# Kernel tuning notes

Measured on AMD Instinct MI355X. Metric: run time of the kernel, lower is better.

Reference implementation:

```python
import jax, jax.numpy as jnp
import numpy as np
from functools import partial

WIDTH = 2560
LRU = 2560
HEADS = 8
DCONV = 4
B = 4
L = 2048


def setup_inputs() -> dict:
    key = jax.random.key(0)
    ks = jax.random.split(key, 16)
    bw = LRU // HEADS
    x = jax.random.normal(ks[0], (B, L, WIDTH), dtype=jnp.float32)
    segment_pos = jnp.broadcast_to(jnp.arange(L, dtype=jnp.int32), (B, L))
    # indices of the last DCONV frames of the left-padded conv input (length L+DCONV-1)
    base = (jnp.arange(DCONV, dtype=jnp.int32) + (L - 1))
    conv_idx = jnp.broadcast_to(base, (B, LRU, DCONV))
    s = 0.02
    return {
        "x": x,
        "segment_pos": segment_pos,
        "conv_idx": conv_idx,
        "Wx": jax.random.normal(ks[1], (LRU, WIDTH), jnp.float32) * s,
        "bx": jax.random.normal(ks[2], (LRU,), jnp.float32) * s,
        "Wy": jax.random.normal(ks[3], (LRU, WIDTH), jnp.float32) * s,
        "conv_w": jax.random.normal(ks[4], (LRU, DCONV), jnp.float32) * s,  # depthwise kernel
        "conv_b": jax.random.normal(ks[5], (LRU,), jnp.float32) * s,
        "gx_w": jax.random.normal(ks[6], (HEADS, bw, bw), jnp.float32) * s,
        "gx_b": jax.random.normal(ks[7], (HEADS, bw), jnp.float32) * s,
        "ga_w": jax.random.normal(ks[8], (HEADS, bw, bw), jnp.float32) * s,
        "ga_b": jax.random.normal(ks[9], (HEADS, bw), jnp.float32) * s,
        "a_param": jax.random.normal(ks[10], (LRU,), jnp.float32),
        "y_bias": jax.random.normal(ks[11], (1, 1, LRU), jnp.float32) * s,
        "Wout": jax.random.normal(ks[12], (WIDTH, LRU), jnp.float32) * s,
        "bout": jax.random.normal(ks[13], (WIDTH,), jnp.float32) * s,
    }


def _block_diag(x, w):
    # x: [B,L,(h*i)], w: [h,i,j] -> [B,L,(h*j)]
    b, l, _ = x.shape
    h, bw, _ = w.shape
    xb = x.reshape(b, l, h, bw)
    y = jnp.einsum('blhi,hij->blhj', xb, w)
    return y.reshape(b, l, h * bw)


def _scan_op(c1, c2):
    a1, b1 = c1
    a2, b2 = c2
    return (a1 * a2, a2 * b1 + b2)


def reference(x, segment_pos, conv_idx, Wx, bx, Wy, conv_w, conv_b,
              gx_w, gx_b, ga_w, ga_b, a_param, y_bias, Wout, bout):
    dc = conv_w.shape[1]
    seqlen = x.shape[1]

    y = jnp.einsum('bld,ed->ble', x, Wy)                 # linear_y (no bias)
    xl = jnp.einsum('bld,ed->ble', x, Wx) + bx           # linear_x

    # causal depthwise conv1d, padding dc-1 on the left, keep first seqlen
    xpad = jnp.pad(xl, ((0, 0), (dc - 1, 0), (0, 0)))    # [B, L+dc-1, LRU]
    xc = conv_b + sum(conv_w[:, k] * xpad[:, k:k + seqlen, :] for k in range(dc))

    # conv_state: gather of padded (channels-first) input at conv_idx
    conv_state = jnp.take_along_axis(xpad.transpose(0, 2, 1), conv_idx.astype(jnp.int32), axis=2)

    gx = _block_diag(xc, gx_w)  # fuse_bias=True: bias added inside rg_lru
    ga = _block_diag(xc, ga_w)

    # rg_lru_ref
    reset = (segment_pos == 0).astype(x.dtype)[..., None]        # [B,L,1]
    gate_x = jax.nn.sigmoid(gx + gx_b.reshape(-1))
    gate_a = jax.nn.sigmoid(ga + ga_b.reshape(-1))
    c = -8.0 * jax.nn.softplus(a_param)
    log_a = c * gate_a
    a = jnp.exp(log_a) * (1.0 - reset)
    multiplier = jnp.sqrt(1.0 - jnp.exp(2.0 * log_a))
    multiplier = reset + (1.0 - reset) * multiplier
    normalized_x = xc * gate_x * multiplier

    _, h = jax.lax.associative_scan(_scan_op, (a, normalized_x), axis=1)
    last_h = h[:, -1]

    out = h * jax.nn.gelu(y + y_bias, approximate=False)
    out = jnp.einsum('ble,de->bld', out, Wout) + bout    # linear_out
    return out, conv_state, last_h
```

## Files before the change

### kernel.cpp

```cpp
#include <hip/hip_runtime.h>
#include <hip/hip_bf16.h>

#define WIDTH_ 2560
#define LRU_   2560
#define HEADS_ 8
#define BW_    320
#define DCONV_ 4
#define BB     4
#define LL     2048
#define MROWS  (BB*LL)
#define NCH    32
#define CLEN   (LL/NCH)

typedef unsigned short ushort_t;
typedef __attribute__((ext_vector_type(8))) short short8;
typedef __attribute__((ext_vector_type(4))) float f32x4;

__device__ __forceinline__ unsigned short f2bf(float f) {
  union { float f; unsigned u; } v; v.f = f;
  unsigned r = v.u + 0x7fffu + ((v.u >> 16) & 1u);
  return (unsigned short)(r >> 16);
}
__device__ __forceinline__ float bf2f(unsigned short h) {
  union { unsigned u; float f; } v; v.u = ((unsigned)h) << 16;
  return v.f;
}
__device__ __forceinline__ void async_load16(const void* g, void* l) {
  __builtin_amdgcn_global_load_lds(
      (const __attribute__((address_space(1))) unsigned*)g,
      (__attribute__((address_space(3))) unsigned*)l, 16, 0, 0);
}
__device__ __forceinline__ float sigmoidf_(float x) {
  return 1.f / (1.f + __expf(-x));
}
__device__ __forceinline__ size_t pkaddr(int e, int m, int PL) {
  return ((size_t)(e >> 3) * PL + m) * 8 + (e & 7);
}

__global__ void tp_pack(const float* __restrict__ src, ushort_t* __restrict__ dst,
                        int R, int C, int PL, int RO) {
  __shared__ float tile[64][65];
  const int r0 = blockIdx.x * 64, c0 = blockIdx.y * 64;
  const int t = threadIdx.x;
#pragma unroll
  for (int it = 0; it < 4; ++it) {
    int row = it * 16 + (t >> 4);
    int col = (t & 15) * 4;
    *(float4*)&tile[row][col] = *(const float4*)&src[(size_t)(r0 + row) * C + c0 + col];
  }
  __syncthreads();
#pragma unroll
  for (int it = 0; it < 2; ++it) {
    int c8 = it * 4 + (t >> 6);
    int m  = t & 63;
    ushort_t o[8];
#pragma unroll
    for (int j = 0; j < 8; ++j) o[j] = f2bf(tile[m][c8 * 8 + j]);
    *(short8*)&dst[((size_t)(c0 / 8 + c8) * PL + RO + r0 + m) * 8] = *(short8*)o;
  }
}

__global__ void gw_pack(const float* __restrict__ w, ushort_t* __restrict__ dst,
                        int RO, int n_) {
  int i = blockIdx.x * blockDim.x + threadIdx.x;
  if (i >= n_) return;
  int n = i % BW_;
  int k = (i / BW_) % BW_;
  int h = i / (BW_ * BW_);
  dst[((size_t)(h * 40 + (k >> 3)) * 640 + RO + n) * 8 + (k & 7)] =
      f2bf(w[((size_t)h * BW_ + k) * BW_ + n]);
}

__global__ void ctab_kernel(const float* __restrict__ apar, float* __restrict__ ctab) {
  int e = blockIdx.x * blockDim.x + threadIdx.x;
  if (e >= LRU_) return;
  float ap = apar[e];
  float sp = (ap > 15.f) ? ap : log1pf(expf(ap));
  ctab[e] = -8.f * sp;
}

template<int EPI>
__global__ __launch_bounds__(512, 2)
void gemm_pk(const ushort_t* __restrict__ A,
             const ushort_t* __restrict__ B, int NPL,
             void* __restrict__ C0, void* __restrict__ C1,
             const float* __restrict__ bias) {
  constexpr int NT = 80;
  __shared__ char smem[131072];
  const int tid = threadIdx.x;
  const int lane = tid & 63, w = tid >> 6;
  const int wr = w >> 2, wc = w & 3;
  const int l15 = lane & 15, l4 = lane >> 4;

  const int nblk = gridDim.x;
  const int TN = nblk >> 5;
  const int x8 = blockIdx.x & 7, c = blockIdx.x >> 3;
  const int tm = (x8 * 4 + c / TN) * 256;
  const int tn = (c % TN) * 256;

  const char* aS[2]; const char* bS[2]; int ld[2];
#pragma unroll
  for (int u = 0; u < 2; ++u) {
    int lb = (u * 512 + tid) * 16;
    int slot = lb >> 12, m = (lb >> 4) & 255;
    aS[u] = (const char*)A + ((size_t)slot * MROWS + tm + m) * 16;
    bS[u] = (const char*)B + ((size_t)slot * NPL + tn + m) * 16;
    ld[u] = lb;
  }
  const size_t aStep = (size_t)4 * MROWS * 16;
  const size_t bStep = (size_t)4 * NPL * 16;

  f32x4 acc[8][4] = {};

#pragma unroll
  for (int kt = 0; kt < 3; ++kt)
#pragma unroll
    for (int u = 0; u < 2; ++u) {
      async_load16(aS[u] + kt * aStep, smem + kt * 16384 + ld[u]);
      async_load16(bS[u] + kt * bStep, smem + 65536 + kt * 16384 + ld[u]);
    }

  const int aRd = l4 * 4096 + (wr * 128 + l15) * 16;
  const int bRd = 65536 + l4 * 4096 + (wc * 64 + l15) * 16;

  for (int t = 0; t < NT; ++t) {
    if (t < NT - 2)       asm volatile("s_waitcnt vmcnt(8)" ::: "memory");
    else if (t == NT - 2) asm volatile("s_waitcnt vmcnt(4)" ::: "memory");
    else                  asm volatile("s_waitcnt vmcnt(0)" ::: "memory");
    __builtin_amdgcn_s_barrier();
    if (t + 3 < NT) {
      const int kt = t + 3, p = kt & 3;
#pragma unroll
      for (int u = 0; u < 2; ++u) {
        async_load16(aS[u] + kt * aStep, smem + p * 16384 + ld[u]);
        async_load16(bS[u] + kt * bStep, smem + 65536 + p * 16384 + ld[u]);
      }
    }
    const char* base = smem + (t & 3) * 16384;
    short8 bfrag[4], afrag[4];
#pragma unroll
    for (int nf = 0; nf < 4; ++nf)
      bfrag[nf] = *(const short8*)(base + bRd + nf * 256);
#pragma unroll
    for (int mf = 0; mf < 4; ++mf)
      afrag[mf] = *(const short8*)(base + aRd + mf * 256);
    __builtin_amdgcn_s_setprio(1);
#pragma unroll
    for (int mf = 0; mf < 4; ++mf)
#pragma unroll
      for (int nf = 0; nf < 4; ++nf)
        acc[mf][nf] = __builtin_amdgcn_mfma_f32_16x16x32_bf16(
            afrag[mf], bfrag[nf], acc[mf][nf], 0, 0, 0);
    __builtin_amdgcn_s_setprio(0);
#pragma unroll
    for (int mf = 0; mf < 4; ++mf)
      afrag[mf] = *(const short8*)(base + aRd + 1024 + mf * 256);
    __builtin_amdgcn_s_setprio(1);
#pragma unroll
    for (int mf = 0; mf < 4; ++mf)
#pragma unroll
      for (int nf = 0; nf < 4; ++nf)
        acc[4 + mf][nf] = __builtin_amdgcn_mfma_f32_16x16x32_bf16(
            afrag[mf], bfrag[nf], acc[4 + mf][nf], 0, 0, 0);
    __builtin_amdgcn_s_setprio(0);
  }

  const int crow0 = tm + wr * 128 + l4 * 4;
  const int ccol0 = tn + wc * 64 + l15;
#pragma unroll
  for (int m = 0; m < 8; ++m)
#pragma unroll
    for (int n = 0; n < 4; ++n) {
      const int col = ccol0 + n * 16;
#pragma unroll
      for (int r = 0; r < 4; ++r) {
        const int row = crow0 + m * 16 + r;
        float v = acc[m][n][r];
        if (EPI == 0) {
          ((float*)C0)[(size_t)row * 2560 + col] = v + bias[col];
        } else {
          if (col < 2560)
            ((ushort_t*)C0)[pkaddr(col, row, MROWS)] = f2bf(v + bias[col]);
          else
            ((ushort_t*)C1)[pkaddr(col - 2560, row, MROWS)] = f2bf(v);
        }
      }
    }
}

__global__ __launch_bounds__(256, 2)
void gate_gemm(const ushort_t* __restrict__ A,
               const ushort_t* __restrict__ Bw,
               ushort_t* __restrict__ GX,
               ushort_t* __restrict__ AAo,
               const float* __restrict__ gxb, const float* __restrict__ gab,
               const float* __restrict__ ctab, const int* __restrict__ seg) {
  constexpr int BM = 128, BN = 64, NF = 2;
  __shared__ char smem[12288];
  const int tid = threadIdx.x;
  const int w = tid >> 6, lane = tid & 63;
  const int wr = w >> 1, wc = w & 1;
  const int l15 = lane & 15, l4 = lane >> 4;
  const int tm = blockIdx.x * BM;
  const int tn = blockIdx.y * BN;
  const int z = blockIdx.z;

  const char* aS[2]; int lda_[2];
#pragma unroll
  for (int u = 0; u < 2; ++u) {
    int lb = (u * 256 + tid) * 16;
    int slot = lb >> 11, m = (lb >> 4) & 127;
    aS[u] = (const char*)A + ((size_t)(z * 40 + slot) * MROWS + tm + m) * 16;
    lda_[u] = lb;
  }
  const char* bS; int ldb_;
  {
    int lb = tid * 16;
    int slot = lb >> 10, n = (lb >> 4) & 63;
    bS = (const char*)Bw + ((size_t)(z * 40 + slot) * 640 + tn + n) * 16;
    ldb_ = 8192 + lb;
  }
  const size_t aStep = (size_t)4 * MROWS * 16;
  const size_t bStep = (size_t)4 * 640 * 16;

  f32x4 acc[4][NF] = {};
  const int aRd = l4 * 2048 + (wr * 64 + l15) * 16;
  const int bRd = 8192 + l4 * 1024 + (wc * 32 + l15) * 16;

  for (int kt = 0; kt < 10; ++kt) {
#pragma unroll
    for (int u = 0; u < 2; ++u)
      async_load16(aS[u] + kt * aStep, smem + lda_[u]);
    async_load16(bS + kt * bStep, smem + ldb_);
    __syncthreads();
    short8 af[4], bfr[NF];
#pragma unroll
    for (int mf = 0; mf < 4; ++mf)
      af[mf] = *(const short8*)(smem + aRd + mf * 256);
#pragma unroll
    for (int nf = 0; nf < NF; ++nf)
      bfr[nf] = *(const short8*)(smem + bRd + nf * 256);
#pragma unroll
    for (int mf = 0; mf < 4; ++mf)
#pragma unroll
      for (int nf = 0; nf < NF; ++nf)
        acc[mf][nf] = __builtin_amdgcn_mfma_f32_16x16x32_bf16(af[mf], bfr[nf], acc[mf][nf], 0, 0, 0);
    __syncthreads();
  }

  const int crow0 = tm + wr * 64 + l4 * 4;
  const int ccol0 = tn + wc * 32 + l15;
#pragma unroll
  for (int mf = 0; mf < 4; ++mf) {
#pragma unroll
    for (int nf = 0; nf < NF; ++nf) {
      const int cih = ccol0 + nf * 16;
#pragma unroll
      for (int r = 0; r < 4; ++r) {
        const int row = crow0 + mf * 16 + r;
        if (cih < BW_) {
          const int gc = z * BW_ + cih;
          float v = acc[mf][nf][r] + gxb[gc];
          float xc = bf2f(A[pkaddr(gc, row, MROWS)]);
          GX[pkaddr(gc, row, MROWS)] = f2bf(xc * sigmoidf_(v));
        } else {
          const int gc = z * BW_ + cih - BW_;
          float v = acc[mf][nf][r] + gab[gc];
          float la = ctab[gc] * sigmoidf_(v);
          float av = (seg[row] == 0) ? 0.f : expf(la);
          AAo[pkaddr(gc, row, MROWS)] = f2bf(av);
        }
      }
    }
  }
}

__global__ void conv_pk(const ushort_t* __restrict__ xl, const float* __restrict__ convw,
                        const float* __restrict__ convb, ushort_t* __restrict__ xc) {
  int i = blockIdx.x * blockDim.x + threadIdx.x;
  if (i >= 320 * MROWS) return;
  int m = i % MROWS;
  int p = i / MROWS;
  int t = m % LL;
  const ushort_t* pl = xl + (size_t)p * MROWS * 8;
  short8 v0 = {}, v1 = {}, v2 = {}, v3;
  v3 = *(const short8*)(pl + (size_t)m * 8);
  if (t >= 1) v2 = *(const short8*)(pl + (size_t)(m - 1) * 8);
  if (t >= 2) v1 = *(const short8*)(pl + (size_t)(m - 2) * 8);
  if (t >= 3) v0 = *(const short8*)(pl + (size_t)(m - 3) * 8);
  ushort_t o[8];
#pragma unroll
  for (int u = 0; u < 8; ++u) {
    int e = p * 8 + u;
    float4 wv = ((const float4*)convw)[e];
    float acc = convb[e];
    acc += wv.x * bf2f((ushort_t)v0[u]);
    acc += wv.y * bf2f((ushort_t)v1[u]);
    acc += wv.z * bf2f((ushort_t)v2[u]);
    acc += wv.w * bf2f((ushort_t)v3[u]);
    o[u] = f2bf(acc);
  }
  *(short8*)(xc + (size_t)p * MROWS * 8 + (size_t)m * 8) = *(short8*)o;
}

__global__ void conv_state_kernel(const ushort_t* __restrict__ xl, const int* __restrict__ cidx,
                                  float* __restrict__ cs) {
  int i = blockIdx.x * blockDim.x + threadIdx.x;
  if (i >= BB * LRU_ * DCONV_) return;
  int e = (i / DCONV_) % LRU_;
  int b = i / (DCONV_ * LRU_);
  int idx = cidx[i];
  int ts = idx - (DCONV_ - 1);
  float v = 0.f;
  if (ts >= 0 && ts < LL) v = bf2f(xl[pkaddr(e, b * LL + ts, MROWS)]);
  cs[i] = v;
}

__global__ void scanA(const ushort_t* __restrict__ AA, const ushort_t* __restrict__ GX,
                      float* __restrict__ cA, float* __restrict__ cH) {
  int i = blockIdx.x * blockDim.x + threadIdx.x;
  if (i >= BB * NCH * LRU_) return;
  int e = i % LRU_;
  int c = (i / LRU_) % NCH;
  int b = i / (LRU_ * NCH);
  float Ap = 1.f, h = 0.f;
  size_t base = pkaddr(e, b * LL + c * CLEN, MROWS);
  for (int t = 0; t < CLEN; ++t) {
    size_t j = base + (size_t)t * 8;
    float a = bf2f(AA[j]);
    float nx = bf2f(GX[j]) * sqrtf(fmaxf(0.f, 1.f - a * a));
    Ap *= a;
    h = a * h + nx;
  }
  cA[i] = Ap; cH[i] = h;
}

__global__ void scanB(const float* __restrict__ cA, const float* __restrict__ cH,
                      float* __restrict__ hInit) {
  int i = blockIdx.x * blockDim.x + threadIdx.x;
  if (i >= BB * LRU_) return;
  int e = i % LRU_;
  int b = i / LRU_;
  float h = 0.f;
  for (int c = 0; c < NCH; ++c) {
    size_t j = ((size_t)b * NCH + c) * LRU_ + e;
    hInit[j] = h;
    h = cA[j] * h + cH[j];
  }
}

__global__ void scanC(const ushort_t* __restrict__ AA, const ushort_t* __restrict__ GXpre,
                      const float* __restrict__ hInit, const ushort_t* __restrict__ ybf,
                      const float* __restrict__ ybias, float* __restrict__ lastH) {
  int i = blockIdx.x * blockDim.x + threadIdx.x;
  if (i >= BB * NCH * LRU_) return;
  int e = i % LRU_;
  int c = (i / LRU_) % NCH;
  int b = i / (LRU_ * NCH);
  float h = hInit[i];
  float yb = ybias[e];
  ushort_t* pre = (ushort_t*)GXpre;
  size_t base = pkaddr(e, b * LL + c * CLEN, MROWS);
  for (int t = 0; t < CLEN; ++t) {
    size_t j = base + (size_t)t * 8;
    float a = bf2f(AA[j]);
    float nx = bf2f(GXpre[j]) * sqrtf(fmaxf(0.f, 1.f - a * a));
    h = a * h + nx;
    float yv = bf2f(ybf[j]) + yb;
    float g = 0.5f * yv * (1.f + erff(yv * 0.70710678118f));
    pre[j] = f2bf(h * g);
  }
  if (c == NCH - 1) lastH[(size_t)b * LRU_ + e] = h;
}

extern "C" void kernel_launch(void* const* d_in, const int* in_sizes, int n_in,
                              void* d_out, int out_size, void* d_ws, size_t ws_size,
                              hipStream_t stream) {
  const float* x     = (const float*)d_in[0];
  const int*   seg   = (const int*)d_in[1];
  const int*   cidx  = (const int*)d_in[2];
  const float* Wx    = (const float*)d_in[3];
  const float* bx    = (const float*)d_in[4];
  const float* Wy    = (const float*)d_in[5];
  const float* convw = (const float*)d_in[6];
  const float* convb = (const float*)d_in[7];
  const float* gxw   = (const float*)d_in[8];
  const float* gxb   = (const float*)d_in[9];
  const float* gaw   = (const float*)d_in[10];
  const float* gab   = (const float*)d_in[11];
  const float* apar  = (const float*)d_in[12];
  const float* ybias = (const float*)d_in[13];
  const float* Wout  = (const float*)d_in[14];
  const float* bout  = (const float*)d_in[15];

  float* out    = (float*)d_out;
  float* cs_out = out + (size_t)MROWS * WIDTH_;
  float* lh_out = cs_out + (size_t)BB * LRU_ * DCONV_;

  ushort_t* ybf = (ushort_t*)d_out;
  ushort_t* AA  = (ushort_t*)((char*)d_out + (size_t)41943040);

  const size_t SZ_BIG = (size_t)MROWS * LRU_ * 2;
  const size_t SZ_WC  = (size_t)(2 * LRU_) * WIDTH_ * 2;
  const size_t SZ_GW  = (size_t)HEADS_ * 640 * BW_ * 2;
  const size_t SZ_SM  = (size_t)BB * NCH * LRU_ * 4;
  size_t need = SZ_BIG * 3 + SZ_WC + SZ_GW + 10240 + SZ_SM * 3;
  if (ws_size < need) return;

  char* p = (char*)d_ws;
  ushort_t* xpk   = (ushort_t*)p; p += SZ_BIG;
  ushort_t* wpk   = (ushort_t*)p; p += SZ_WC;
  ushort_t* T2    = (ushort_t*)p; p += SZ_BIG;
  ushort_t* xcbf  = (ushort_t*)p; p += SZ_BIG;
  ushort_t* gwT   = (ushort_t*)p; p += SZ_GW;
  float*    ctab  = (float*)p;    p += 10240;
  float*    cA    = (float*)p;    p += SZ_SM;
  float*    cH    = (float*)p;    p += SZ_SM;
  float*    hInit = (float*)p;    p += SZ_SM;
  ushort_t* woutpk = wpk;

  const int BLK = 256;
  tp_pack<<<dim3(MROWS / 64, WIDTH_ / 64), 256, 0, stream>>>(x, xpk, MROWS, WIDTH_, MROWS, 0);
  tp_pack<<<dim3(LRU_ / 64, WIDTH_ / 64), 256, 0, stream>>>(Wx, wpk, LRU_, WIDTH_, 2 * LRU_, 0);
  tp_pack<<<dim3(LRU_ / 64, WIDTH_ / 64), 256, 0, stream>>>(Wy, wpk, LRU_, WIDTH_, 2 * LRU_, LRU_);

  gemm_pk<1><<<640, 512, 0, stream>>>(xpk, wpk, 2 * LRU_, T2, ybf, bx);

  tp_pack<<<dim3(LRU_ / 64, WIDTH_ / 64), 256, 0, stream>>>(Wout, woutpk, WIDTH_, LRU_, WIDTH_, 0);

  conv_pk<<<(320 * MROWS + BLK - 1) / BLK, BLK, 0, stream>>>(T2, convw, convb, xcbf);
  conv_state_kernel<<<(BB * LRU_ * DCONV_ + BLK - 1) / BLK, BLK, 0, stream>>>(T2, cidx, cs_out);

  gw_pack<<<(HEADS_ * BW_ * BW_ + BLK - 1) / BLK, BLK, 0, stream>>>(gxw, gwT, 0, HEADS_ * BW_ * BW_);
  gw_pack<<<(HEADS_ * BW_ * BW_ + BLK - 1) / BLK, BLK, 0, stream>>>(gaw, gwT, BW_, HEADS_ * BW_ * BW_);
  ctab_kernel<<<(LRU_ + BLK - 1) / BLK, BLK, 0, stream>>>(apar, ctab);

  gate_gemm<<<dim3(MROWS / 128, 10, HEADS_), BLK, 0, stream>>>(
      xcbf, gwT, T2, AA, gxb, gab, ctab, seg);

  scanA<<<(BB * NCH * LRU_ + BLK - 1) / BLK, BLK, 0, stream>>>(AA, T2, cA, cH);
  scanB<<<(BB * LRU_ + BLK - 1) / BLK, BLK, 0, stream>>>(cA, cH, hInit);
  scanC<<<(BB * NCH * LRU_ + BLK - 1) / BLK, BLK, 0, stream>>>(AA, T2, hInit, ybf, ybias, lh_out);

  gemm_pk<0><<<320, 512, 0, stream>>>(T2, woutpk, WIDTH_, out, nullptr, bout);
}
```

Baseline: 591.8 us.

## Restructure big GEMM main loop into 8-phase K=64 double-buffered pipeline

Rewrites the main loop of the 256x256 bf16 GEMM to use K=64 steps, split into half-tiles, with double buffering. Each step runs four phases that interleave LDS fragment reads, async global staging of the next A/B halves, and MFMA bursts, separated by sched_barriers and workgroup barriers. B fragments are reused across the four A-quarter phases. The aim is better overlap of global loads and LDS reads with MFMA and fewer loop iterations, at the cost of more barriers per K-step and more register pressure. The gate_gemm edit only inlines a constant.

```diff
diff --git a/kernel.cpp b/kernel.cpp
--- a/kernel.cpp
+++ b/kernel.cpp
@@ -79,18 +79,59 @@
   ctab[e] = -8.f * sp;
 }
 
+
+#define STG_A(KT, H, BUF) do { \
+  _Pragma("unroll") for (int u_ = 0; u_ < 2; ++u_) \
+    async_load16(Ach + aoff[u_] + (size_t)(KT) * aKt + (H) * 2048, \
+                 smem + ((BUF) * 2 + (H)) * 16384 + ldst[u_]); } while (0)
+#define STG_B(KT, H, BUF) do { \
+  _Pragma("unroll") for (int u_ = 0; u_ < 2; ++u_) \
+    async_load16(Bch + boff[u_] + (size_t)(KT) * bKt + (H) * 2048, \
+                 smem + 65536 + ((BUF) * 2 + (H)) * 16384 + ldst[u_]); } while (0)
+
+#define PHASE(BUF, Q, STAGE_STMT, VMN) do { \
+  __builtin_amdgcn_sched_barrier(0); \
+  const char* Ah_ = smem + ((BUF) * 2 + wr) * 16384; \
+  const char* Bh_ = smem + 65536 + ((BUF) * 2 + (wc >> 1)) * 16384; \
+  if ((Q) == 0) { \
+    _Pragma("unroll") for (int nf = 0; nf < 4; ++nf) \
+      _Pragma("unroll") for (int s = 0; s < 2; ++s) \
+        bfr[nf][s] = *(const short8*)(Bh_ + ((s * 4 + l4) * 128 + brow + nf * 16 + l15) * 16); \
+  } \
+  short8 a_[2][2]; \
+  _Pragma("unroll") for (int mm = 0; mm < 2; ++mm) \
+    _Pragma("unroll") for (int s = 0; s < 2; ++s) \
+      a_[mm][s] = *(const short8*)(Ah_ + ((s * 4 + l4) * 128 + ((Q) * 2 + mm) * 16 + l15) * 16); \
+  STAGE_STMT; \
+  __builtin_amdgcn_sched_barrier(0); \
+  __builtin_amdgcn_s_barrier(); \
+  asm volatile("s_waitcnt lgkmcnt(0)" ::: "memory"); \
+  __builtin_amdgcn_sched_barrier(0); \
+  __builtin_amdgcn_s_setprio(1); \
+  _Pragma("unroll") for (int mm = 0; mm < 2; ++mm) \
+    _Pragma("unroll") for (int nf = 0; nf < 4; ++nf) \
+      _Pragma("unroll") for (int s = 0; s < 2; ++s) \
+        acc[(Q) * 2 + mm][nf] = __builtin_amdgcn_mfma_f32_16x16x32_bf16( \
+            a_[mm][s], bfr[nf][s], acc[(Q) * 2 + mm][nf], 0, 0, 0); \
+  __builtin_amdgcn_s_setprio(0); \
+  if ((VMN) == 4)      asm volatile("s_waitcnt vmcnt(4)" ::: "memory"); \
+  else if ((VMN) == 0) asm volatile("s_waitcnt vmcnt(0)" ::: "memory"); \
+  __builtin_amdgcn_sched_barrier(0); \
+  __builtin_amdgcn_s_barrier(); \
+} while (0)
+
 template<int EPI>
 __global__ __launch_bounds__(512, 2)
 void gemm_pk(const ushort_t* __restrict__ A,
              const ushort_t* __restrict__ B, int NPL,
              void* __restrict__ C0, void* __restrict__ C1,
              const float* __restrict__ bias) {
-  constexpr int NT = 80;
   __shared__ char smem[131072];
   const int tid = threadIdx.x;
   const int lane = tid & 63, w = tid >> 6;
   const int wr = w >> 2, wc = w & 3;
   const int l15 = lane & 15, l4 = lane >> 4;
+  const int brow = (wc & 1) * 64;
 
   const int nblk = gridDim.x;
   const int TN = nblk >> 5;
@@ -98,71 +139,42 @@
   const int tm = (x8 * 4 + c / TN) * 256;
   const int tn = (c % TN) * 256;
 
-  const char* aS[2]; const char* bS[2]; int ld[2];
+  const char* Ach = (const char*)A;
+  const char* Bch = (const char*)B;
+  const size_t aKt = (size_t)8 * MROWS * 16;
+  const size_t bKt = (size_t)8 * NPL * 16;
+
+  size_t aoff[2], boff[2]; int ldst[2];
 #pragma unroll
   for (int u = 0; u < 2; ++u) {
     int lb = (u * 512 + tid) * 16;
-    int slot = lb >> 12, m = (lb >> 4) & 255;
-    aS[u] = (const char*)A + ((size_t)slot * MROWS + tm + m) * 16;
-    bS[u] = (const char*)B + ((size_t)slot * NPL + tn + m) * 16;
-    ld[u] = lb;
-  }
-  const size_t aStep = (size_t)4 * MROWS * 16;
-  const size_t bStep = (size_t)4 * NPL * 16;
+    int slot = lb >> 11, m = (lb >> 4) & 127;
+    aoff[u] = ((size_t)slot * MROWS + tm + m) * 16;
+    boff[u] = ((size_t)slot * NPL + tn + m) * 16;
+    ldst[u] = lb;
+  }
 
   f32x4 acc[8][4] = {};
-
-#pragma unroll
-  for (int kt = 0; kt < 3; ++kt)
-#pragma unroll
-    for (int u = 0; u < 2; ++u) {
-      async_load16(aS[u] + kt * aStep, smem + kt * 16384 + ld[u]);
-      async_load16(bS[u] + kt * bStep, smem + 65536 + kt * 16384 + ld[u]);
-    }
-
-  const int aRd = l4 * 4096 + (wr * 128 + l15) * 16;
-  const int bRd = 65536 + l4 * 4096 + (wc * 64 + l15) * 16;
-
-  for (int t = 0; t < NT; ++t) {
-    if (t < NT - 2)       asm volatile("s_waitcnt vmcnt(8)" ::: "memory");
-    else if (t == NT - 2) asm volatile("s_waitcnt vmcnt(4)" ::: "memory");
-    else                  asm volatile("s_waitcnt vmcnt(0)" ::: "memory");
-    __builtin_amdgcn_s_barrier();
-    if (t + 3 < NT) {
-      const int kt = t + 3, p = kt & 3;
-#pragma unroll
-      for (int u = 0; u < 2; ++u) {
-        async_load16(aS[u] + kt * aStep, smem + p * 16384 + ld[u]);
-        async_load16(bS[u] + kt * bStep, smem + 65536 + p * 16384 + ld[u]);
-      }
-    }
-    const char* base = smem + (t & 3) * 16384;
-    short8 bfrag[4], afrag[4];
-#pragma unroll
-    for (int nf = 0; nf < 4; ++nf)
-      bfrag[nf] = *(const short8*)(base + bRd + nf * 256);
-#pragma unroll
-    for (int mf = 0; mf < 4; ++mf)
-      afrag[mf] = *(const short8*)(base + aRd + mf * 256);
-    __builtin_amdgcn_s_setprio(1);
-#pragma unroll
-    for (int mf = 0; mf < 4; ++mf)
-#pragma unroll
-      for (int nf = 0; nf < 4; ++nf)
-        acc[mf][nf] = __builtin_amdgcn_mfma_f32_16x16x32_bf16(
-            afrag[mf], bfrag[nf], acc[mf][nf], 0, 0, 0);
-    __builtin_amdgcn_s_setprio(0);
-#pragma unroll
-    for (int mf = 0; mf < 4; ++mf)
-      afrag[mf] = *(const short8*)(base + aRd + 1024 + mf * 256);
-    __builtin_amdgcn_s_setprio(1);
-#pragma unroll
-    for (int mf = 0; mf < 4; ++mf)
-#pragma unroll
-      for (int nf = 0; nf < 4; ++nf)
-        acc[4 + mf][nf] = __builtin_amdgcn_mfma_f32_16x16x32_bf16(
-            afrag[mf], bfrag[nf], acc[4 + mf][nf], 0, 0, 0);
-    __builtin_amdgcn_s_setprio(0);
+  short8 bfr[4][2];
+
+  STG_B(0, 0, 0); STG_B(0, 1, 0); STG_A(0, 0, 0); STG_A(0, 1, 0);
+  STG_B(1, 0, 1); STG_B(1, 1, 1);
+  asm volatile("s_waitcnt vmcnt(4)" ::: "memory");
+  __builtin_amdgcn_sched_barrier(0);
+  __builtin_amdgcn_s_barrier();
+
+#pragma unroll 1
+  for (int i = 0; i < 20; ++i) {
+    const int k1 = 2 * i + 1, k2 = 2 * i + 2, k3 = 2 * i + 3;
+    const bool v2 = (k2 < 40), v3 = (k3 < 40);
+    PHASE(0, 0, STG_A(k1, 0, 1), -1);
+    PHASE(0, 1, STG_A(k1, 1, 1), -1);
+    PHASE(0, 2, if (v2) STG_B(k2, 0, 0), -1);
+    PHASE(0, 3, if (v2) STG_B(k2, 1, 0), (v2 ? 4 : 0));
+    PHASE(1, 0, if (v2) STG_A(k2, 0, 0), -1);
+    PHASE(1, 1, if (v2) STG_A(k2, 1, 0), -1);
+    PHASE(1, 2, if (v3) STG_B(k3, 0, 1), -1);
+    PHASE(1, 3, if (v3) STG_B(k3, 1, 1), (v3 ? 4 : (v2 ? 0 : -1)));
   }
 
   const int crow0 = tm + wr * 128 + l4 * 4;
@@ -195,14 +207,14 @@
                ushort_t* __restrict__ AAo,
                const float* __restrict__ gxb, const float* __restrict__ gab,
                const float* __restrict__ ctab, const int* __restrict__ seg) {
-  constexpr int BM = 128, BN = 64, NF = 2;
+  constexpr int BM = 128, NF = 2;
   __shared__ char smem[12288];
   const int tid = threadIdx.x;
   const int w = tid >> 6, lane = tid & 63;
   const int wr = w >> 1, wc = w & 1;
   const int l15 = lane & 15, l4 = lane >> 4;
   const int tm = blockIdx.x * BM;
-  const int tn = blockIdx.y * BN;
+  const int tn = blockIdx.y * 64;
   const int z = blockIdx.z;
 
   const char* aS[2]; int lda_[2];
```

Result: faster. 572.7 us (-3.2%).
